# Optimization experiments

Measured on AMD Instinct MI355X. Metric: run time of the kernel, lower is better.

The kernel has to match this reference:

```python
import jax, jax.numpy as jnp
import numpy as np

# Edge-type spec: (src_node_type, dst_node_type); 0=argument, 1=evidence
REL_SPEC = ((0, 0), (1, 0), (0, 1))


def _hgt_layer(xs, edges, Wk, bk, Wq, bq, Wv, bv, a_rel, m_rel, p_rel, Wa, ba, skip):
    # xs: list of [N_t, C]; edges: tuple of [2, E] int arrays per edge type
    H, D = a_rel.shape[1], a_rel.shape[2]
    Ns = [x.shape[0] for x in xs]
    k = [(xs[t] @ Wk[t] + bk[t]).reshape(Ns[t], H, D) for t in range(len(xs))]
    q = [(xs[t] @ Wq[t] + bq[t]).reshape(Ns[t], H, D) for t in range(len(xs))]
    v = [(xs[t] @ Wv[t] + bv[t]).reshape(Ns[t], H, D) for t in range(len(xs))]
    scale = 1.0 / jnp.sqrt(jnp.asarray(D, xs[0].dtype))
    agg = [jnp.zeros((n, H, D), xs[0].dtype) for n in Ns]
    for r, (s, d) in enumerate(REL_SPEC):
        src, dst = edges[r][0], edges[r][1]
        # relation-specific key/message transforms, per edge: [E, H, D]
        k_e = jnp.einsum('ehd,hdf->ehf', k[s][src], a_rel[r])
        v_e = jnp.einsum('ehd,hdf->ehf', v[s][src], m_rel[r])
        alpha = jnp.einsum('ehd,ehd->eh', q[d][dst], k_e) * p_rel[r] * scale  # [E, H]
        # segment softmax over incoming edges of each destination node
        amax = jax.ops.segment_max(alpha, dst, num_segments=Ns[d])
        a_exp = jnp.exp(alpha - amax[dst])
        denom = jax.ops.segment_sum(a_exp, dst, num_segments=Ns[d])
        w = a_exp / jnp.maximum(denom[dst], 1e-16)
        agg[d] = agg[d] + jax.ops.segment_sum(v_e * w[..., None], dst, num_segments=Ns[d])
    out = []
    for t in range(len(xs)):
        o = jax.nn.gelu(agg[t].reshape(Ns[t], H * D), approximate=False) @ Wa[t] + ba[t]
        beta = jax.nn.sigmoid(skip[t])
        out.append(beta * o + (1.0 - beta) * xs[t])
    return out


def setup_inputs() -> dict:
    key = jax.random.key(0)
    N_ARG, N_EV, F_IN, C, H, L, E = 50000, 50000, 64, 128, 8, 2, 500000
    D = C // H
    R, T = 3, 2  # edge types, node types
    ks = jax.random.split(key, 20)
    s_in = 1.0 / np.sqrt(F_IN)
    s_c = 1.0 / np.sqrt(C)
    s_d = 1.0 / np.sqrt(D)
    inp = {
        'x_arg': jax.random.normal(ks[0], (N_ARG, F_IN), jnp.float32),
        'x_ev': jax.random.normal(ks[1], (N_EV, F_IN), jnp.float32),
        'edge_aa': jax.random.randint(ks[2], (2, E), 0, N_ARG, jnp.int32),
        'edge_ea': jax.random.randint(ks[3], (2, E), 0, N_EV, jnp.int32),
        'edge_ae': jax.random.randint(ks[4], (2, E), 0, N_ARG, jnp.int32),
        'Win_arg': jax.random.normal(ks[5], (F_IN, C), jnp.float32) * s_in,
        'bin_arg': jnp.zeros((C,), jnp.float32),
        'Win_ev': jax.random.normal(ks[6], (F_IN, C), jnp.float32) * s_in,
        'bin_ev': jnp.zeros((C,), jnp.float32),
        'Wk': jax.random.normal(ks[7], (L, T, C, C), jnp.float32) * s_c,
        'bk': jnp.zeros((L, T, C), jnp.float32),
        'Wq': jax.random.normal(ks[8], (L, T, C, C), jnp.float32) * s_c,
        'bq': jnp.zeros((L, T, C), jnp.float32),
        'Wv': jax.random.normal(ks[9], (L, T, C, C), jnp.float32) * s_c,
        'bv': jnp.zeros((L, T, C), jnp.float32),
        'a_rel': jax.random.normal(ks[10], (L, R, H, D, D), jnp.float32) * s_d,
        'm_rel': jax.random.normal(ks[11], (L, R, H, D, D), jnp.float32) * s_d,
        'p_rel': jnp.ones((L, R, H), jnp.float32),
        'Wa': jax.random.normal(ks[12], (L, T, C, C), jnp.float32) * s_c,
        'ba': jnp.zeros((L, T, C), jnp.float32),
        'skip': jnp.ones((L, T), jnp.float32),
        'Wc1': jax.random.normal(ks[13], (C, C), jnp.float32) * s_c,
        'bc1': jnp.zeros((C,), jnp.float32),
        'Wc2': jax.random.normal(ks[14], (C, 1), jnp.float32) * s_c,
        'bc2': jnp.zeros((1,), jnp.float32),
    }
    return inp


def reference(x_arg, x_ev, edge_aa, edge_ea, edge_ae, Win_arg, bin_arg, Win_ev, bin_ev,
              Wk, bk, Wq, bq, Wv, bv, a_rel, m_rel, p_rel, Wa, ba, skip,
              Wc1, bc1, Wc2, bc2):
    # type-specific input projections + relu
    h = [jax.nn.relu(x_arg @ Win_arg + bin_arg), jax.nn.relu(x_ev @ Win_ev + bin_ev)]
    edges = (edge_aa, edge_ea, edge_ae)
    for l in range(Wk.shape[0]):
        h = _hgt_layer(h, edges, Wk[l], bk[l], Wq[l], bq[l], Wv[l], bv[l],
                       a_rel[l], m_rel[l], p_rel[l], Wa[l], ba[l], skip[l])
    g = jnp.mean(h[0], axis=0, keepdims=True)  # [1, C]
    z = jax.nn.relu(g @ Wc1 + bc1)
    return jax.nn.sigmoid(z @ Wc2 + bc2)  # [1, 1]
```

## Files before the change

kernel.cpp:

```cpp
#include <hip/hip_runtime.h>
#include <hip/hip_fp8.h>
#include <math.h>

typedef __attribute__((ext_vector_type(8))) short short8v;
typedef __attribute__((ext_vector_type(4))) float f32x4;
typedef __attribute__((ext_vector_type(2))) float f32x2;

__device__ __forceinline__ float bf2f(unsigned short u) {
    union { unsigned int i; float f; } x; x.i = ((unsigned int)u) << 16; return x.f;
}
__device__ __forceinline__ unsigned short f2bf(float f) {
    union { float f; unsigned int i; } x; x.f = f;
    unsigned int r = x.i + 0x7fffu + ((x.i >> 16) & 1u);
    return (unsigned short)(r >> 16);
}
__device__ __forceinline__ unsigned int pk_bf16(float lo, float hi) {
    unsigned int r;
    asm("v_cvt_pk_bf16_f32 %0, %1, %2" : "=v"(r) : "v"(lo), "v"(hi));
    return r;
}
__device__ __forceinline__ unsigned int pk_fp8x4(float v0, float v1, float v2, float v3) {
    int pk = __builtin_amdgcn_cvt_pk_fp8_f32(v0, v1, 0, false);
    pk = __builtin_amdgcn_cvt_pk_fp8_f32(v2, v3, pk, true);
    return (unsigned int)pk;
}
__device__ __forceinline__ float gelu_exact(float x) {
    return 0.5f * x * (1.0f + erff(x * 0.70710678118654752f));
}

template <int K, int MODE, int ASRC>
__device__ __forceinline__ void gemm_body(
    const void* __restrict__ Aptr, const unsigned short* __restrict__ BT,
    const float* __restrict__ bias, unsigned short* __restrict__ Cout, int M,
    const unsigned short* __restrict__ hprev, const float* __restrict__ skipp, int blk) {
    __shared__ short As[128 * K];
    const int tid = threadIdx.x;
    const int row0 = blk * 128;
    const int CH = K / 8;

#pragma unroll
    for (int i = 0; i < (128 * CH) / 256; ++i) {
        int idx = tid + i * 256;
        int r = idx / CH, c = idx % CH;
        int gr = row0 + r;
        if (ASRC == 0) {
            short8v val = {0, 0, 0, 0, 0, 0, 0, 0};
            if (gr < M)
                val = *reinterpret_cast<const short8v*>(
                    (const unsigned short*)Aptr + (size_t)gr * K + c * 8);
            if (MODE == 2) {
                float fv[8];
#pragma unroll
                for (int u = 0; u < 8; ++u) fv[u] = gelu_exact(bf2f((unsigned short)val[u]));
                uint4 uu;
                uu.x = pk_bf16(fv[0], fv[1]);
                uu.y = pk_bf16(fv[2], fv[3]);
                uu.z = pk_bf16(fv[4], fv[5]);
                uu.w = pk_bf16(fv[6], fv[7]);
                *reinterpret_cast<uint4*>((char*)As + r * (2 * K) +
                                          ((c * 16) ^ ((r & 7) << 4))) = uu;
            } else {
                *reinterpret_cast<short8v*>((char*)As + r * (2 * K) +
                                            ((c * 16) ^ ((r & 7) << 4))) = val;
            }
        } else {
            uint4 u = make_uint4(0u, 0u, 0u, 0u);
            if (gr < M) {
                const float* Af = (const float*)Aptr;
                float4 f0 = *reinterpret_cast<const float4*>(Af + (size_t)gr * K + c * 8);
                float4 f1 = *reinterpret_cast<const float4*>(Af + (size_t)gr * K + c * 8 + 4);
                u.x = pk_bf16(f0.x, f0.y);
                u.y = pk_bf16(f0.z, f0.w);
                u.z = pk_bf16(f1.x, f1.y);
                u.w = pk_bf16(f1.z, f1.w);
            }
            *reinterpret_cast<uint4*>((char*)As + r * (2 * K) + ((c * 16) ^ ((r & 7) << 4))) = u;
        }
    }
    __syncthreads();

    const int lane = tid & 63, wid = tid >> 6;
    const int wr = wid >> 1, wc = wid & 1;
    const int lr = lane & 15, lg = lane >> 4;
    const int swz = (lr & 7) << 4;
    const unsigned short* bbase = BT + (size_t)(wc * 64 + lr) * K + lg * 8;
    f32x4 acc[4][4];
    f32x4 z4 = {0.f, 0.f, 0.f, 0.f};
#pragma unroll
    for (int mi = 0; mi < 4; ++mi)
#pragma unroll
        for (int ni = 0; ni < 4; ++ni) acc[mi][ni] = z4;

#pragma unroll
    for (int ks = 0; ks < K / 32; ++ks) {
        int kc = ks * 64 + lg * 16;
        short8v a[4], b[4];
#pragma unroll
        for (int ni = 0; ni < 4; ++ni)
            b[ni] = *reinterpret_cast<const short8v*>(bbase + (size_t)ni * 16 * K + ks * 32);
#pragma unroll
        for (int mi = 0; mi < 4; ++mi) {
            int r = wr * 64 + mi * 16 + lr;
            a[mi] = *reinterpret_cast<const short8v*>((char*)As + r * (2 * K) + (kc ^ swz));
        }
#pragma unroll
        for (int mi = 0; mi < 4; ++mi)
#pragma unroll
            for (int ni = 0; ni < 4; ++ni)
                acc[mi][ni] =
                    __builtin_amdgcn_mfma_f32_16x16x32_bf16(b[ni], a[mi], acc[mi][ni], 0, 0, 0);
    }

    float beta = 0.f;
    if (MODE == 2) beta = 1.f / (1.f + expf(-skipp[0]));
#pragma unroll
    for (int mi = 0; mi < 4; ++mi) {
        int gr = row0 + wr * 64 + mi * 16 + lr;
        if (gr >= M) continue;
#pragma unroll
        for (int ni = 0; ni < 4; ++ni) {
            int col0 = wc * 64 + ni * 16 + lg * 4;
            float4 bv = *reinterpret_cast<const float4*>(bias + col0);
            float v0 = acc[mi][ni][0] + bv.x;
            float v1 = acc[mi][ni][1] + bv.y;
            float v2 = acc[mi][ni][2] + bv.z;
            float v3 = acc[mi][ni][3] + bv.w;
            if (MODE == 1) {
                v0 = fmaxf(v0, 0.f); v1 = fmaxf(v1, 0.f);
                v2 = fmaxf(v2, 0.f); v3 = fmaxf(v3, 0.f);
            }
            if (MODE == 2) {
                ushort4 hp = *reinterpret_cast<const ushort4*>(hprev + (size_t)gr * 128 + col0);
                float ob = 1.f - beta;
                v0 = beta * v0 + ob * bf2f(hp.x);
                v1 = beta * v1 + ob * bf2f(hp.y);
                v2 = beta * v2 + ob * bf2f(hp.z);
                v3 = beta * v3 + ob * bf2f(hp.w);
            }
            uint2 us;
            us.x = pk_bf16(v0, v1);
            us.y = pk_bf16(v2, v3);
            *reinterpret_cast<uint2*>(Cout + (size_t)gr * 128 + col0) = us;
        }
    }
}

template <int K, int MODE, int ASRC>
__global__ __launch_bounds__(256) void gemm_dual(
    const void* A0, const unsigned short* BT0, const float* b0, unsigned short* C0, int M0,
    const unsigned short* hp0, const float* sk0,
    const void* A1, const unsigned short* BT1, const float* b1, unsigned short* C1, int M1,
    const unsigned short* hp1, const float* sk1, int nb0) {
    if ((int)blockIdx.x < nb0)
        gemm_body<K, MODE, ASRC>(A0, BT0, b0, C0, M0, hp0, sk0, blockIdx.x);
    else
        gemm_body<K, MODE, ASRC>(A1, BT1, b1, C1, M1, hp1, sk1, blockIdx.x - nb0);
}

struct QKVJobs {
    const unsigned short* BT[5];
    const float* bias[5];
    unsigned short* outBf[5];
    unsigned char* outF8[5];
    int f8off[5];
};

template <int NB>
__device__ __forceinline__ void qkv_body(short* __restrict__ As,
                                         const unsigned short* __restrict__ A,
                                         const QKVJobs& J, int M, int blk) {
    const int tid = threadIdx.x;
    const int row0 = blk * 128;

#pragma unroll
    for (int i = 0; i < 8; ++i) {
        int idx = tid + i * 256;
        int r = idx >> 4, c = idx & 15;
        int gr = row0 + r;
        short8v val = {0, 0, 0, 0, 0, 0, 0, 0};
        if (gr < M) val = *reinterpret_cast<const short8v*>(A + (size_t)gr * 128 + c * 8);
        *reinterpret_cast<short8v*>((char*)As + r * 256 + ((c * 16) ^ ((r & 7) << 4))) = val;
    }
    __syncthreads();

    const int lane = tid & 63, wid = tid >> 6;
    const int wr = wid >> 1, wc = wid & 1;
    const int lr = lane & 15, lg = lane >> 4;
    const int swz = (lr & 7) << 4;

    short8v a[4][4];
#pragma unroll
    for (int ks = 0; ks < 4; ++ks) {
        int kc = ks * 64 + lg * 16;
#pragma unroll
        for (int mi = 0; mi < 4; ++mi) {
            int r = wr * 64 + mi * 16 + lr;
            a[ks][mi] = *reinterpret_cast<const short8v*>((char*)As + r * 256 + (kc ^ swz));
        }
    }

#pragma unroll
    for (int m = 0; m < NB; ++m) {
        const unsigned short* bbase = J.BT[m] + (size_t)(wc * 64 + lr) * 128 + lg * 8;
        f32x4 acc[4][4];
        f32x4 z4 = {0.f, 0.f, 0.f, 0.f};
#pragma unroll
        for (int mi = 0; mi < 4; ++mi)
#pragma unroll
            for (int ni = 0; ni < 4; ++ni) acc[mi][ni] = z4;

#pragma unroll
        for (int ks = 0; ks < 4; ++ks) {
            short8v b[4];
#pragma unroll
            for (int ni = 0; ni < 4; ++ni)
                b[ni] = *reinterpret_cast<const short8v*>(bbase + (size_t)ni * 16 * 128 + ks * 32);
#pragma unroll
            for (int mi = 0; mi < 4; ++mi)
#pragma unroll
                for (int ni = 0; ni < 4; ++ni)
                    acc[mi][ni] = __builtin_amdgcn_mfma_f32_16x16x32_bf16(b[ni], a[ks][mi],
                                                                          acc[mi][ni], 0, 0, 0);
        }

        unsigned short* outBf = J.outBf[m];
        unsigned char* outF8 = J.outF8[m];
        int off = J.f8off[m];
        const float* bias = J.bias[m];
#pragma unroll
        for (int mi = 0; mi < 4; ++mi) {
            int gr = row0 + wr * 64 + mi * 16 + lr;
            if (gr >= M) continue;
#pragma unroll
            for (int ni = 0; ni < 4; ++ni) {
                int col0 = wc * 64 + ni * 16 + lg * 4;
                float4 bv = *reinterpret_cast<const float4*>(bias + col0);
                float v0 = acc[mi][ni][0] + bv.x;
                float v1 = acc[mi][ni][1] + bv.y;
                float v2 = acc[mi][ni][2] + bv.z;
                float v3 = acc[mi][ni][3] + bv.w;
                if (outBf) {
                    uint2 us;
                    us.x = pk_bf16(v0, v1);
                    us.y = pk_bf16(v2, v3);
                    *reinterpret_cast<uint2*>(outBf + (size_t)gr * 128 + col0) = us;
                } else {
                    *reinterpret_cast<unsigned int*>(outF8 + (size_t)gr * 256 + off + col0) =
                        pk_fp8x4(v0, v1, v2, v3);
                }
            }
        }
    }
}

__global__ __launch_bounds__(256) void gemm_qkv2(const unsigned short* A0, QKVJobs J0, int M0,
                                                 int nb0, const unsigned short* A1,
                                                 QKVJobs J1, int M1) {
    __shared__ short As[128 * 128];
    if ((int)blockIdx.x < nb0) qkv_body<5>(As, A0, J0, M0, blockIdx.x);
    else qkv_body<3>(As, A1, J1, M1, blockIdx.x - nb0);
}

__global__ void convT_kernel(const float* __restrict__ Win0, const float* __restrict__ Win1,
                             const float* __restrict__ Wq, const float* __restrict__ Wa,
                             unsigned short* __restrict__ winT, unsigned short* __restrict__ wqT,
                             unsigned short* __restrict__ waT, int nmat) {
    int gid = blockIdx.x * 256 + threadIdx.x;
    if (gid < 2 * 8192) {
        int m = gid >> 13, idx = gid & 8191;
        int n = idx >> 6, k = idx & 63;
        const float* W = m ? Win1 : Win0;
        winT[gid] = f2bf(W[(size_t)k * 128 + n]);
        return;
    }
    int g = gid - 2 * 8192;
    if (g < nmat * 16384) {
        int mat = g >> 14, idx = g & 16383;
        int n = idx >> 7, k = idx & 127;
        wqT[g] = f2bf(Wq[(size_t)mat * 16384 + (size_t)k * 128 + n]);
        return;
    }
    g -= nmat * 16384;
    if (g < nmat * 16384) {
        int mat = g >> 14, idx = g & 16383;
        int n = idx >> 7, k = idx & 127;
        waT[g] = f2bf(Wa[(size_t)mat * 16384 + (size_t)k * 128 + n]);
    }
}

__global__ void fold_kernel(const float* __restrict__ Wk, const float* __restrict__ bk,
                            const float* __restrict__ Wv, const float* __restrict__ bv,
                            const float* __restrict__ a_rel, const float* __restrict__ m_rel,
                            unsigned short* __restrict__ wfT, float* __restrict__ bfold, int L) {
    const int RSarr[3] = {0, 1, 0};
    int gid = blockIdx.x * 256 + threadIdx.x;
    int NW = L * 6 * 16384;
    if (gid < NW) {
        int fold = gid >> 14, idx = gid & 16383;
        int col = idx >> 7, i = idx & 127;
        int kv = fold & 1, lr = fold >> 1, l = lr / 3, r = lr % 3;
        int s = RSarr[r];
        const float* W = (kv ? Wv : Wk) + (size_t)(l * 2 + s) * 16384;
        const float* rel = (kv ? m_rel : a_rel) + (size_t)(l * 3 + r) * 2048;
        int hh = col >> 4, f = col & 15;
        float sacc = 0.f;
#pragma unroll
        for (int d = 0; d < 16; ++d)
            sacc += W[(size_t)i * 128 + hh * 16 + d] * rel[hh * 256 + d * 16 + f];
        wfT[gid] = f2bf(sacc);
        return;
    }
    int g = gid - NW;
    if (g >= L * 6 * 128) return;
    int fold = g >> 7, col = g & 127;
    int kv = fold & 1, lr = fold >> 1, l = lr / 3, r = lr % 3;
    int s = RSarr[r];
    const float* b = (kv ? bv : bk) + (size_t)(l * 2 + s) * 128;
    const float* rel = (kv ? m_rel : a_rel) + (size_t)(l * 3 + r) * 2048;
    int hh = col >> 4, f = col & 15;
    float sacc = 0.f;
#pragma unroll
    for (int d = 0; d < 16; ++d) sacc += b[hh * 16 + d] * rel[hh * 256 + d * 16 + f];
    bfold[fold * 128 + col] = sacc;
}

struct Csr3 {
    const int* src[3];
    const int* dst[3];
    int E[3];
    int* cnt;
    int* texcl;
    int* bsums;
    int* indptr[3];
    int* ssrc[3];
    int Nd[3];
    int nb[3];
    int stride;
};

__global__ void hist3_kernel(Csr3 P, int Etot) {
    int gid = blockIdx.x * 256 + threadIdx.x;
    if (gid >= Etot) return;
    int r = 0, off = gid;
    if (off >= P.E[0]) { off -= P.E[0]; r = 1; if (off >= P.E[1]) { off -= P.E[1]; r = 2; } }
    atomicAdd(&P.cnt[r * P.stride + P.dst[r][off]], 1);
}

__global__ __launch_bounds__(1024) void scanA3_kernel(Csr3 P) {
    __shared__ int s[1024];
    int b = blockIdx.x, r = 0;
    while (b >= P.nb[r]) { b -= P.nb[r]; ++r; }
    const int* cnt = P.cnt + r * P.stride;
    int* texcl = P.texcl + r * P.stride;
    int n = P.Nd[r];
    int t = threadIdx.x;
    int gid = b * 1024 + t;
    int x = (gid < n) ? cnt[gid] : 0;
    s[t] = x;
    __syncthreads();
    for (int off = 1; off < 1024; off <<= 1) {
        int v = (t >= off) ? s[t - off] : 0;
        __syncthreads();
        s[t] += v;
        __syncthreads();
    }
    if (gid < n) texcl[gid] = s[t] - x;
    if (t == 1023) P.bsums[r * 64 + b] = s[1023];
}

__global__ void scanB3_kernel(Csr3 P) {
    int r = blockIdx.x;
    if (threadIdx.x == 0) {
        int run = 0;
        for (int i = 0; i < P.nb[r]; ++i) {
            int t = P.bsums[r * 64 + i];
            P.bsums[r * 64 + i] = run;
            run += t;
        }
    }
}

__global__ __launch_bounds__(1024) void scanC3_kernel(Csr3 P) {
    int b = blockIdx.x, r = 0;
    while (b >= P.nb[r]) { b -= P.nb[r]; ++r; }
    int n = P.Nd[r];
    int gid = b * 1024 + threadIdx.x;
    if (gid < n) {
        int v = P.texcl[r * P.stride + gid] + P.bsums[r * 64 + b];
        P.indptr[r][gid] = v;
        P.cnt[r * P.stride + gid] = v;
    }
    if (gid == 0) P.indptr[r][n] = P.E[r];
}

__global__ void scatter3_kernel(Csr3 P, int Etot) {
    int gid = blockIdx.x * 256 + threadIdx.x;
    if (gid >= Etot) return;
    int r = 0, off = gid;
    if (off >= P.E[0]) { off -= P.E[0]; r = 1; if (off >= P.E[1]) { off -= P.E[1]; r = 2; } }
    int d = P.dst[r][off];
    int p = atomicAdd(&P.cnt[r * P.stride + d], 1);
    P.ssrc[r][p] = P.src[r][off];
}

__global__ void gcur_init_kernel(Csr3 P, int* __restrict__ gcur) {
    int t = threadIdx.x;
    if (t >= 192) return;
    int r = t >> 6, b = t & 63;
    int nbk = (P.Nd[r] + 1023) >> 10;
    gcur[t] = (b < nbk) ? P.indptr[r][b << 10] : 0;
}

#define PA_TILE 4096
#define PA_BLKS 64
__global__ __launch_bounds__(256) void partA_kernel(Csr3 P, unsigned int* __restrict__ pb0,
                                                    unsigned int* __restrict__ pb1,
                                                    unsigned int* __restrict__ pb2,
                                                    int* __restrict__ gcur) {
    unsigned int* pbuf[3] = {pb0, pb1, pb2};
    const int r = blockIdx.x / PA_BLKS;
    const int blk = blockIdx.x % PA_BLKS;
    const int tid = threadIdx.x;
    const int* __restrict__ srcp = P.src[r];
    const int* __restrict__ dstp = P.dst[r];
    const int E = P.E[r];
    unsigned int* __restrict__ out = pbuf[r];
    __shared__ unsigned int stage[PA_TILE];
    __shared__ unsigned char bkt[PA_TILE];
    __shared__ int lcnt[64], lofs[64], lbase[64];

    for (int t0 = blk * PA_TILE; t0 < E; t0 += PA_BLKS * PA_TILE) {
        int cnt = E - t0;
        if (cnt > PA_TILE) cnt = PA_TILE;
        if (tid < 64) lcnt[tid] = 0;
        __syncthreads();
        unsigned int pk[16];
        int lp[16];
#pragma unroll
        for (int j = 0; j < 16; ++j) {
            int i = tid + j * 256;
            if (i < cnt) {
                int s = srcp[t0 + i];
                int d = dstp[t0 + i];
                pk[j] = ((unsigned int)d << 16) | (unsigned int)s;
                lp[j] = atomicAdd(&lcnt[d >> 10], 1);
            }
        }
        __syncthreads();
        if (tid == 0) {
            int run = 0;
            for (int b = 0; b < 64; ++b) { lofs[b] = run; run += lcnt[b]; }
        }
        __syncthreads();
        if (tid < 64 && lcnt[tid] > 0) lbase[tid] = atomicAdd(&gcur[r * 64 + tid], lcnt[tid]);
        __syncthreads();
#pragma unroll
        for (int j = 0; j < 16; ++j) {
            int i = tid + j * 256;
            if (i < cnt) {
                int b = pk[j] >> 26;
                int sp = lofs[b] + lp[j];
                stage[sp] = pk[j];
                bkt[sp] = (unsigned char)b;
            }
        }
        __syncthreads();
        for (int k = tid; k < cnt; k += 256) {
            int b = bkt[k];
            out[lbase[b] + (k - lofs[b])] = stage[k];
        }
        __syncthreads();
    }
}

__global__ __launch_bounds__(256) void partB_kernel(Csr3 P, const unsigned int* __restrict__ pb0,
                                                    const unsigned int* __restrict__ pb1,
                                                    const unsigned int* __restrict__ pb2) {
    const unsigned int* pbuf[3] = {pb0, pb1, pb2};
    int r = blockIdx.x >> 6, b = blockIdx.x & 63;
    int Nd = P.Nd[r];
    int nbk = (Nd + 1023) >> 10;
    if (b >= nbk) return;
    int d1 = (b + 1) << 10;
    if (d1 > Nd) d1 = Nd;
    int lo = P.indptr[r][b << 10];
    int hi = P.indptr[r][d1];
    const unsigned int* __restrict__ pin = pbuf[r];
    int* __restrict__ cursor = P.cnt + r * P.stride;
    int* __restrict__ out = P.ssrc[r];
    for (int i = lo + (int)threadIdx.x; i < hi; i += 256) {
        unsigned int pk = pin[i];
        int d = pk >> 16;
        int p = atomicAdd(&cursor[d], 1);
        out[p] = (int)(pk & 0xffffu);
    }
}

__device__ __forceinline__ void proc4(uint4 Kw, uint4 Vw, const float qf[16], float ps,
                                      bool valid, float& ssum, float acc[16]) {
    float kx[16];
    {
        f32x2 p0 = __builtin_amdgcn_cvt_pk_f32_fp8(Kw.x, false);
        f32x2 p1 = __builtin_amdgcn_cvt_pk_f32_fp8(Kw.x, true);
        f32x2 p2 = __builtin_amdgcn_cvt_pk_f32_fp8(Kw.y, false);
        f32x2 p3 = __builtin_amdgcn_cvt_pk_f32_fp8(Kw.y, true);
        f32x2 p4 = __builtin_amdgcn_cvt_pk_f32_fp8(Kw.z, false);
        f32x2 p5 = __builtin_amdgcn_cvt_pk_f32_fp8(Kw.z, true);
        f32x2 p6 = __builtin_amdgcn_cvt_pk_f32_fp8(Kw.w, false);
        f32x2 p7 = __builtin_amdgcn_cvt_pk_f32_fp8(Kw.w, true);
        kx[0] = p0[0]; kx[1] = p0[1]; kx[2] = p1[0]; kx[3] = p1[1];
        kx[4] = p2[0]; kx[5] = p2[1]; kx[6] = p3[0]; kx[7] = p3[1];
        kx[8] = p4[0]; kx[9] = p4[1]; kx[10] = p5[0]; kx[11] = p5[1];
        kx[12] = p6[0]; kx[13] = p6[1]; kx[14] = p7[0]; kx[15] = p7[1];
    }
    float t = 0.f;
#pragma unroll
    for (int j = 0; j < 16; ++j) t = fmaf(qf[j], kx[j], t);
    float e = fminf(fmaxf(t * ps, -40.f), 40.f);
    float w = valid ? exp2f(e) : 0.f;
    ssum += w;
    float vx[16];
    {
        f32x2 p0 = __builtin_amdgcn_cvt_pk_f32_fp8(Vw.x, false);
        f32x2 p1 = __builtin_amdgcn_cvt_pk_f32_fp8(Vw.x, true);
        f32x2 p2 = __builtin_amdgcn_cvt_pk_f32_fp8(Vw.y, false);
        f32x2 p3 = __builtin_amdgcn_cvt_pk_f32_fp8(Vw.y, true);
        f32x2 p4 = __builtin_amdgcn_cvt_pk_f32_fp8(Vw.z, false);
        f32x2 p5 = __builtin_amdgcn_cvt_pk_f32_fp8(Vw.z, true);
        f32x2 p6 = __builtin_amdgcn_cvt_pk_f32_fp8(Vw.w, false);
        f32x2 p7 = __builtin_amdgcn_cvt_pk_f32_fp8(Vw.w, true);
        vx[0] = p0[0]; vx[1] = p0[1]; vx[2] = p1[0]; vx[3] = p1[1];
        vx[4] = p2[0]; vx[5] = p2[1]; vx[6] = p3[0]; vx[7] = p3[1];
        vx[8] = p4[0]; vx[9] = p4[1]; vx[10] = p5[0]; vx[11] = p5[1];
        vx[12] = p6[0]; vx[13] = p6[1]; vx[14] = p7[0]; vx[15] = p7[1];
    }
#pragma unroll
    for (int j = 0; j < 16; ++j) acc[j] = fmaf(w, vx[j], acc[j]);
}

__device__ __forceinline__ void slot_load(const unsigned char* __restrict__ kv,
                                          const int* __restrict__ ss, int beg, int n, int j4,
                                          int lq, int lhb, int eslot, int hoff, int& bat,
                                          uint4& Kw, uint4& Vw) {
    if ((j4 & 31) == 0) bat = (j4 + lq < n) ? ss[beg + j4 + lq] : 0;
    int s = __shfl(bat, lhb + ((j4 + eslot) & 31));
    const unsigned char* bp = kv + (size_t)s * 256 + hoff;
    Kw = *reinterpret_cast<const uint4*>(bp);
    Vw = *reinterpret_cast<const uint4*>(bp + 128);
}

__global__ __launch_bounds__(256) void attn_fused(
    const unsigned short* __restrict__ q0, const unsigned short* __restrict__ q1,
    const unsigned char* __restrict__ kvA, const unsigned char* __restrict__ kvB,
    const unsigned char* __restrict__ kvC,
    const int* __restrict__ ipA, const int* __restrict__ ssA,
    const int* __restrict__ ipB, const int* __restrict__ ssB,
    const int* __restrict__ ipC, const int* __restrict__ ssC,
    unsigned short* __restrict__ agg0, unsigned short* __restrict__ agg1,
    const float* __restrict__ prA, const float* __restrict__ prB,
    const float* __restrict__ prC, int N0, int N1) {
    const int wave = (blockIdx.x * blockDim.x + threadIdx.x) >> 6;
    const int lane = threadIdx.x & 63;
    const int lq = lane & 31;
    const int lhb = lane & 32;
    const int h = lq & 7;
    const int eslot = lq >> 3;
    const int hoff = h * 16;
    const float LOG2E = 1.4426950408889634f;
    const int P0 = (N0 + 1) >> 1;
    const int P1 = (N1 + 1) >> 1;
    if (wave >= P0 + P1) return;

    if (wave < P0) {
        int dst = wave * 2 + (lhb >> 5);
        bool act = dst < N0;
        float qf[16];
        int b1 = 0, n1 = 0, b2 = 0, n2 = 0;
        if (act) {
            short8v qv0 = *reinterpret_cast<const short8v*>(q0 + (size_t)dst * 128 + hoff);
            short8v qv1 = *reinterpret_cast<const short8v*>(q0 + (size_t)dst * 128 + hoff + 8);
#pragma unroll
            for (int j = 0; j < 8; ++j) {
                qf[j] = bf2f((unsigned short)qv0[j]);
                qf[8 + j] = bf2f((unsigned short)qv1[j]);
            }
            b1 = ipA[dst]; n1 = ipA[dst + 1] - b1;
            b2 = ipB[dst]; n2 = ipB[dst + 1] - b2;
        } else {
#pragma unroll
            for (int j = 0; j < 16; ++j) qf[j] = 0.f;
        }
        float ps1 = prA[h] * 0.25f * LOG2E;
        float ps2 = prB[h] * 0.25f * LOG2E;
        float ssum1 = 0.f, ssum2 = 0.f;
        float acc1[16], acc2[16];
#pragma unroll
        for (int j = 0; j < 16; ++j) { acc1[j] = 0.f; acc2[j] = 0.f; }
        int it1 = (n1 + 3) >> 2, it2 = (n2 + 3) >> 2;
        int itm = (it1 > it2) ? it1 : it2;
        int bat1 = 0, bat2 = 0;
        uint4 cK1{}, cV1{}, cK2{}, cV2{};
        if (it1 > 0) slot_load(kvA, ssA, b1, n1, 0, lq, lhb, eslot, hoff, bat1, cK1, cV1);
        if (it2 > 0) slot_load(kvB, ssB, b2, n2, 0, lq, lhb, eslot, hoff, bat2, cK2, cV2);
        for (int i = 0; i < itm; ++i) {
            uint4 nK1{}, nV1{}, nK2{}, nV2{};
            if (i + 1 < it1)
                slot_load(kvA, ssA, b1, n1, (i + 1) * 4, lq, lhb, eslot, hoff, bat1, nK1, nV1);
            if (i + 1 < it2)
                slot_load(kvB, ssB, b2, n2, (i + 1) * 4, lq, lhb, eslot, hoff, bat2, nK2, nV2);
            if (i < it1) proc4(cK1, cV1, qf, ps1, (i * 4 + eslot) < n1, ssum1, acc1);
            if (i < it2) proc4(cK2, cV2, qf, ps2, (i * 4 + eslot) < n2, ssum2, acc2);
            cK1 = nK1; cV1 = nV1; cK2 = nK2; cV2 = nV2;
        }
#pragma unroll
        for (int j = 0; j < 16; ++j) {
            acc1[j] += __shfl_xor(acc1[j], 8);
            acc1[j] += __shfl_xor(acc1[j], 16);
            acc2[j] += __shfl_xor(acc2[j], 8);
            acc2[j] += __shfl_xor(acc2[j], 16);
        }
        ssum1 += __shfl_xor(ssum1, 8);
        ssum1 += __shfl_xor(ssum1, 16);
        ssum2 += __shfl_xor(ssum2, 8);
        ssum2 += __shfl_xor(ssum2, 16);
        if (act && eslot == 0) {
            float i1 = 1.f / fmaxf(ssum1, 1e-16f);
            float i2 = 1.f / fmaxf(ssum2, 1e-16f);
            float v[16];
#pragma unroll
            for (int j = 0; j < 16; ++j) v[j] = acc1[j] * i1 + acc2[j] * i2;
            unsigned short* op = agg0 + (size_t)dst * 128 + hoff;
            uint4 w0, w1;
            w0.x = pk_bf16(v[0], v[1]);  w0.y = pk_bf16(v[2], v[3]);
            w0.z = pk_bf16(v[4], v[5]);  w0.w = pk_bf16(v[6], v[7]);
            w1.x = pk_bf16(v[8], v[9]);  w1.y = pk_bf16(v[10], v[11]);
            w1.z = pk_bf16(v[12], v[13]); w1.w = pk_bf16(v[14], v[15]);
            *reinterpret_cast<uint4*>(op) = w0;
            *reinterpret_cast<uint4*>(op + 8) = w1;
        }
    } else {
        int dst = (wave - P0) * 2 + (lhb >> 5);
        bool act = dst < N1;
        float qf[16];
        int b1 = 0, n1 = 0;
        if (act) {
            short8v qv0 = *reinterpret_cast<const short8v*>(q1 + (size_t)dst * 128 + hoff);
            short8v qv1 = *reinterpret_cast<const short8v*>(q1 + (size_t)dst * 128 + hoff + 8);
#pragma unroll
            for (int j = 0; j < 8; ++j) {
                qf[j] = bf2f((unsigned short)qv0[j]);
                qf[8 + j] = bf2f((unsigned short)qv1[j]);
            }
            b1 = ipC[dst]; n1 = ipC[dst + 1] - b1;
        } else {
#pragma unroll
            for (int j = 0; j < 16; ++j) qf[j] = 0.f;
        }
        float ps1 = prC[h] * 0.25f * LOG2E;
        float ssum1 = 0.f;
        float acc1[16];
#pragma unroll
        for (int j = 0; j < 16; ++j) acc1[j] = 0.f;
        int it1 = (n1 + 3) >> 2;
        int bat1 = 0;
        uint4 cK1{}, cV1{};
        if (it1 > 0) slot_load(kvC, ssC, b1, n1, 0, lq, lhb, eslot, hoff, bat1, cK1, cV1);
        for (int i = 0; i < it1; ++i) {
            uint4 nK1{}, nV1{};
            if (i + 1 < it1)
                slot_load(kvC, ssC, b1, n1, (i + 1) * 4, lq, lhb, eslot, hoff, bat1, nK1, nV1);
            proc4(cK1, cV1, qf, ps1, (i * 4 + eslot) < n1, ssum1, acc1);
            cK1 = nK1; cV1 = nV1;
        }
#pragma unroll
        for (int j = 0; j < 16; ++j) {
            acc1[j] += __shfl_xor(acc1[j], 8);
            acc1[j] += __shfl_xor(acc1[j], 16);
        }
        ssum1 += __shfl_xor(ssum1, 8);
        ssum1 += __shfl_xor(ssum1, 16);
        if (act && eslot == 0) {
            float i1 = 1.f / fmaxf(ssum1, 1e-16f);
            float v[16];
#pragma unroll
            for (int j = 0; j < 16; ++j) v[j] = acc1[j] * i1;
            unsigned short* op = agg1 + (size_t)dst * 128 + hoff;
            uint4 w0, w1;
            w0.x = pk_bf16(v[0], v[1]);  w0.y = pk_bf16(v[2], v[3]);
            w0.z = pk_bf16(v[4], v[5]);  w0.w = pk_bf16(v[6], v[7]);
            w1.x = pk_bf16(v[8], v[9]);  w1.y = pk_bf16(v[10], v[11]);
            w1.z = pk_bf16(v[12], v[13]); w1.w = pk_bf16(v[14], v[15]);
            *reinterpret_cast<uint4*>(op) = w0;
            *reinterpret_cast<uint4*>(op + 8) = w1;
        }
    }
}

__global__ void colsum_kernel(const unsigned short* __restrict__ h, float* __restrict__ gsum,
                              int M) {
    int c = threadIdx.x;
    float s = 0.f;
    for (int r = blockIdx.x; r < M; r += gridDim.x) s += bf2f(h[(size_t)r * 128 + c]);
    atomicAdd(&gsum[c], s);
}

__global__ void final_kernel(const float* __restrict__ gsum, const float* __restrict__ Wc1,
                             const float* __restrict__ bc1, const float* __restrict__ Wc2,
                             const float* __restrict__ bc2, float* __restrict__ out,
                             float invM) {
    __shared__ float g[128];
    __shared__ float red[128];
    int t = threadIdx.x;
    g[t] = gsum[t] * invM;
    __syncthreads();
    float acc = bc1[t];
    for (int k = 0; k < 128; ++k) acc += g[k] * Wc1[k * 128 + t];
    float zv = fmaxf(acc, 0.f);
    red[t] = zv * Wc2[t];
    __syncthreads();
    for (int off = 64; off > 0; off >>= 1) {
        if (t < off) red[t] += red[t + off];
        __syncthreads();
    }
    if (t == 0) out[0] = 1.f / (1.f + expf(-(red[0] + bc2[0])));
}

extern "C" void kernel_launch(void* const* d_in, const int* in_sizes, int n_in,
                              void* d_out, int out_size, void* d_ws, size_t ws_size,
                              hipStream_t stream) {
    const float* x[2] = {(const float*)d_in[0], (const float*)d_in[1]};
    const int* edges[3] = {(const int*)d_in[2], (const int*)d_in[3], (const int*)d_in[4]};
    const float* Win[2] = {(const float*)d_in[5], (const float*)d_in[7]};
    const float* bin[2] = {(const float*)d_in[6], (const float*)d_in[8]};
    const float* Wk = (const float*)d_in[9];
    const float* bk = (const float*)d_in[10];
    const float* Wq = (const float*)d_in[11];
    const float* bq = (const float*)d_in[12];
    const float* Wv = (const float*)d_in[13];
    const float* bv = (const float*)d_in[14];
    const float* a_rel = (const float*)d_in[15];
    const float* m_rel = (const float*)d_in[16];
    const float* p_rel = (const float*)d_in[17];
    const float* Wa = (const float*)d_in[18];
    const float* ba = (const float*)d_in[19];
    const float* skip = (const float*)d_in[20];
    const float* Wc1 = (const float*)d_in[21];
    const float* bc1 = (const float*)d_in[22];
    const float* Wc2 = (const float*)d_in[23];
    const float* bc2 = (const float*)d_in[24];

    const int N0 = in_sizes[0] / 64;
    const int N1 = in_sizes[1] / 64;
    const int L = in_sizes[9] / (2 * 128 * 128);
    const int Ns[2] = {N0, N1};
    const int RD[3] = {0, 0, 1};
    const int Nmax = (N0 > N1) ? N0 : N1;

    char* p = (char*)d_ws;
    auto alloc = [&](size_t bytes) -> void* {
        void* r = (void*)p;
        p += (bytes + 255) & ~(size_t)255;
        return r;
    };
    unsigned short* h[2];
    unsigned short* q[2];
    unsigned short* agg[2];
    h[0] = (unsigned short*)alloc((size_t)N0 * 128 * 2);
    h[1] = (unsigned short*)alloc((size_t)N1 * 128 * 2);
    q[0] = (unsigned short*)alloc((size_t)N0 * 128 * 2);
    q[1] = (unsigned short*)alloc((size_t)N1 * 128 * 2);
    agg[0] = (unsigned short*)alloc((size_t)N0 * 128 * 2);
    agg[1] = (unsigned short*)alloc((size_t)N1 * 128 * 2);
    unsigned char* kv8[3];
    for (int r = 0; r < 3; ++r) kv8[r] = (unsigned char*)alloc((size_t)Nmax * 256);
    int* indptr[3];
    int* ssrc[3];
    int Er[3];
    for (int r = 0; r < 3; ++r) {
        Er[r] = in_sizes[2 + r] / 2;
        indptr[r] = (int*)alloc((size_t)(Ns[RD[r]] + 1) * 4);
        ssrc[r] = (int*)alloc((size_t)Er[r] * 4);
    }
    unsigned int* pbuf[3];
    for (int r = 0; r < 3; ++r) pbuf[r] = (unsigned int*)alloc((size_t)Er[r] * 4);
    int* cnt3 = (int*)alloc((size_t)3 * Nmax * 4);
    int* texcl3 = (int*)alloc((size_t)3 * Nmax * 4);
    int* bsums3 = (int*)alloc(3 * 64 * 4);
    int* gcur = (int*)alloc(3 * 64 * 4);
    unsigned short* winT = (unsigned short*)alloc(2 * 8192 * 2);
    unsigned short* wqT = (unsigned short*)alloc((size_t)L * 2 * 16384 * 2);
    unsigned short* waT = (unsigned short*)alloc((size_t)L * 2 * 16384 * 2);
    unsigned short* wfT = (unsigned short*)alloc((size_t)L * 6 * 16384 * 2);
    float* bfold = (float*)alloc((size_t)L * 6 * 128 * 4);
    float* gsum = (float*)alloc(128 * 4);

    {
        int nmat = L * 2;
        int convN = 2 * 8192 + 2 * nmat * 16384;
        convT_kernel<<<(convN + 255) / 256, 256, 0, stream>>>(Win[0], Win[1], Wq, Wa, winT, wqT,
                                                              waT, nmat);
        int foldN = L * 6 * 16384 + L * 6 * 128;
        fold_kernel<<<(foldN + 255) / 256, 256, 0, stream>>>(Wk, bk, Wv, bv, a_rel, m_rel, wfT,
                                                             bfold, L);
    }

    {
        Csr3 P;
        int Etot = 0;
        int nbTot = 0;
        for (int r = 0; r < 3; ++r) {
            P.src[r] = edges[r];
            P.dst[r] = edges[r] + Er[r];
            P.E[r] = Er[r];
            P.indptr[r] = indptr[r];
            P.ssrc[r] = ssrc[r];
            P.Nd[r] = Ns[RD[r]];
            P.nb[r] = (P.Nd[r] + 1023) / 1024;
            Etot += Er[r];
            nbTot += P.nb[r];
        }
        P.cnt = cnt3;
        P.texcl = texcl3;
        P.bsums = bsums3;
        P.stride = Nmax;
        hipMemsetAsync(cnt3, 0, (size_t)3 * Nmax * 4, stream);
        hist3_kernel<<<(Etot + 255) / 256, 256, 0, stream>>>(P, Etot);
        scanA3_kernel<<<nbTot, 1024, 0, stream>>>(P);
        scanB3_kernel<<<3, 64, 0, stream>>>(P);
        scanC3_kernel<<<nbTot, 1024, 0, stream>>>(P);
        if (Nmax <= 65536) {
            gcur_init_kernel<<<1, 256, 0, stream>>>(P, gcur);
            partA_kernel<<<3 * PA_BLKS, 256, 0, stream>>>(P, pbuf[0], pbuf[1], pbuf[2], gcur);
            partB_kernel<<<3 * 64, 256, 0, stream>>>(P, pbuf[0], pbuf[1], pbuf[2]);
        } else {
            scatter3_kernel<<<(Etot + 255) / 256, 256, 0, stream>>>(P, Etot);
        }
    }

    const int nb0 = (N0 + 127) / 128, nb1 = (N1 + 127) / 128;

    gemm_dual<64, 1, 1><<<nb0 + nb1, 256, 0, stream>>>(
        x[0], winT, bin[0], h[0], N0, nullptr, nullptr,
        x[1], winT + 8192, bin[1], h[1], N1, nullptr, nullptr, nb0);

    for (int l = 0; l < L; ++l) {
        {
            QKVJobs J0{};
            J0.BT[0] = wqT + (size_t)(l * 2 + 0) * 16384;
            J0.bias[0] = bq + (size_t)(l * 2 + 0) * 128;
            J0.outBf[0] = q[0]; J0.outF8[0] = nullptr; J0.f8off[0] = 0;
            int fk0 = (l * 3 + 0) * 2, fk2 = (l * 3 + 2) * 2;
            J0.BT[1] = wfT + (size_t)fk0 * 16384;       J0.bias[1] = bfold + (size_t)fk0 * 128;
            J0.outBf[1] = nullptr; J0.outF8[1] = kv8[0]; J0.f8off[1] = 0;
            J0.BT[2] = wfT + (size_t)(fk0 + 1) * 16384; J0.bias[2] = bfold + (size_t)(fk0 + 1) * 128;
            J0.outBf[2] = nullptr; J0.outF8[2] = kv8[0]; J0.f8off[2] = 128;
            J0.BT[3] = wfT + (size_t)fk2 * 16384;       J0.bias[3] = bfold + (size_t)fk2 * 128;
            J0.outBf[3] = nullptr; J0.outF8[3] = kv8[2]; J0.f8off[3] = 0;
            J0.BT[4] = wfT + (size_t)(fk2 + 1) * 16384; J0.bias[4] = bfold + (size_t)(fk2 + 1) * 128;
            J0.outBf[4] = nullptr; J0.outF8[4] = kv8[2]; J0.f8off[4] = 128;
            QKVJobs J1{};
            J1.BT[0] = wqT + (size_t)(l * 2 + 1) * 16384;
            J1.bias[0] = bq + (size_t)(l * 2 + 1) * 128;
            J1.outBf[0] = q[1]; J1.outF8[0] = nullptr; J1.f8off[0] = 0;
            int fk1 = (l * 3 + 1) * 2;
            J1.BT[1] = wfT + (size_t)fk1 * 16384;       J1.bias[1] = bfold + (size_t)fk1 * 128;
            J1.outBf[1] = nullptr; J1.outF8[1] = kv8[1]; J1.f8off[1] = 0;
            J1.BT[2] = wfT + (size_t)(fk1 + 1) * 16384; J1.bias[2] = bfold + (size_t)(fk1 + 1) * 128;
            J1.outBf[2] = nullptr; J1.outF8[2] = kv8[1]; J1.f8off[2] = 128;
            gemm_qkv2<<<nb0 + nb1, 256, 0, stream>>>(h[0], J0, N0, nb0, h[1], J1, N1);
        }
        {
            int waves = ((N0 + 1) >> 1) + ((N1 + 1) >> 1);
            attn_fused<<<(waves + 3) / 4, 256, 0, stream>>>(
                q[0], q[1], kv8[0], kv8[1], kv8[2], indptr[0], ssrc[0], indptr[1], ssrc[1],
                indptr[2], ssrc[2], agg[0], agg[1], p_rel + (size_t)(l * 3 + 0) * 8,
                p_rel + (size_t)(l * 3 + 1) * 8, p_rel + (size_t)(l * 3 + 2) * 8, N0, N1);
        }
        gemm_dual<128, 2, 0><<<nb0 + nb1, 256, 0, stream>>>(
            agg[0], waT + (size_t)(l * 2 + 0) * 16384, ba + (size_t)(l * 2 + 0) * 128, h[0], N0,
            h[0], skip + (size_t)(l * 2 + 0),
            agg[1], waT + (size_t)(l * 2 + 1) * 16384, ba + (size_t)(l * 2 + 1) * 128, h[1], N1,
            h[1], skip + (size_t)(l * 2 + 1), nb0);
    }

    hipMemsetAsync(gsum, 0, 128 * 4, stream);
    colsum_kernel<<<512, 128, 0, stream>>>(h[0], gsum, N0);
    final_kernel<<<1, 128, 0, stream>>>(gsum, Wc1, bc1, Wc2, bc2, (float*)d_out,
                                        1.0f / (float)N0);
}
```

Measured before the change: 571.4 us.

## Replace global histogram and scan CSR build with bucketed counting sort

For the small-graph path, CSR construction no longer runs a full per-node global histogram with atomics followed by a three-pass scan. It counts edges per 1024-node bucket with shared-memory atomics, scans the 64 bucket totals in a single thread, and partitions edges by bucket. Each partB block then builds its own local histogram and scan in shared memory to write indptr, and scatters sources using shared-memory atomics. This removes the large memset and the global atomic traffic, at the cost of one extra pass over the dst array and a serial scan kernel.

```diff
diff --git a/kernel.cpp b/kernel.cpp
--- a/kernel.cpp
+++ b/kernel.cpp
@@ -403,12 +403,39 @@
     P.ssrc[r][p] = P.src[r][off];
 }
 
-__global__ void gcur_init_kernel(Csr3 P, int* __restrict__ gcur) {
-    int t = threadIdx.x;
-    if (t >= 192) return;
-    int r = t >> 6, b = t & 63;
-    int nbk = (P.Nd[r] + 1023) >> 10;
-    gcur[t] = (b < nbk) ? P.indptr[r][b << 10] : 0;
+#define CA_TILE 4096
+__global__ __launch_bounds__(256) void countA_kernel(Csr3 P, int* __restrict__ gbkt) {
+    const int r = blockIdx.x >> 6;
+    const int blk = blockIdx.x & 63;
+    const int tid = threadIdx.x;
+    const int* __restrict__ dstp = P.dst[r];
+    const int E = P.E[r];
+    __shared__ int lc[64];
+    for (int t0 = blk * CA_TILE; t0 < E; t0 += 64 * CA_TILE) {
+        int cnt = E - t0;
+        if (cnt > CA_TILE) cnt = CA_TILE;
+        if (tid < 64) lc[tid] = 0;
+        __syncthreads();
+        for (int i = tid; i < cnt; i += 256) atomicAdd(&lc[dstp[t0 + i] >> 10], 1);
+        __syncthreads();
+        if (tid < 64 && lc[tid] > 0) atomicAdd(&gbkt[r * 65 + tid], lc[tid]);
+        __syncthreads();
+    }
+}
+
+__global__ void scanG_kernel(int* __restrict__ gbkt, int* __restrict__ gcur) {
+    if (threadIdx.x == 0) {
+        for (int r = 0; r < 3; ++r) {
+            int run = 0;
+            for (int b = 0; b < 64; ++b) {
+                int t = gbkt[r * 65 + b];
+                gbkt[r * 65 + b] = run;
+                gcur[r * 64 + b] = run;
+                run += t;
+            }
+            gbkt[r * 65 + 64] = run;
+        }
+    }
 }
 
 #define PA_TILE 4096
@@ -473,26 +500,59 @@
     }
 }
 
-__global__ __launch_bounds__(256) void partB_kernel(Csr3 P, const unsigned int* __restrict__ pb0,
-                                                    const unsigned int* __restrict__ pb1,
-                                                    const unsigned int* __restrict__ pb2) {
+__global__ __launch_bounds__(256) void partB2_kernel(Csr3 P, const unsigned int* __restrict__ pb0,
+                                                     const unsigned int* __restrict__ pb1,
+                                                     const unsigned int* __restrict__ pb2,
+                                                     const int* __restrict__ gbkt) {
     const unsigned int* pbuf[3] = {pb0, pb1, pb2};
     int r = blockIdx.x >> 6, b = blockIdx.x & 63;
     int Nd = P.Nd[r];
     int nbk = (Nd + 1023) >> 10;
     if (b >= nbk) return;
-    int d1 = (b + 1) << 10;
+    int d0 = b << 10;
+    int d1 = d0 + 1024;
     if (d1 > Nd) d1 = Nd;
-    int lo = P.indptr[r][b << 10];
-    int hi = P.indptr[r][d1];
+    int lo = gbkt[r * 65 + b];
+    int hi = gbkt[r * 65 + b + 1];
     const unsigned int* __restrict__ pin = pbuf[r];
-    int* __restrict__ cursor = P.cnt + r * P.stride;
+    int* __restrict__ indptr = P.indptr[r];
     int* __restrict__ out = P.ssrc[r];
-    for (int i = lo + (int)threadIdx.x; i < hi; i += 256) {
+    const int tid = threadIdx.x;
+    __shared__ int cnt[1024];
+    __shared__ int exc[1024];
+    __shared__ int ps[256];
+
+    for (int i = tid; i < 1024; i += 256) cnt[i] = 0;
+    __syncthreads();
+    for (int i = lo + tid; i < hi; i += 256)
+        atomicAdd(&cnt[(pin[i] >> 16) & 1023], 1);
+    __syncthreads();
+    int base = tid * 4;
+    int s0 = cnt[base], s1 = cnt[base + 1], s2 = cnt[base + 2], s3 = cnt[base + 3];
+    int tsum = s0 + s1 + s2 + s3;
+    ps[tid] = tsum;
+    __syncthreads();
+    for (int off = 1; off < 256; off <<= 1) {
+        int v = (tid >= off) ? ps[tid - off] : 0;
+        __syncthreads();
+        ps[tid] += v;
+        __syncthreads();
+    }
+    int texc = ps[tid] - tsum;
+    exc[base] = texc;
+    exc[base + 1] = texc + s0;
+    exc[base + 2] = texc + s0 + s1;
+    exc[base + 3] = texc + s0 + s1 + s2;
+    __syncthreads();
+    for (int i = tid; i < (d1 - d0); i += 256) indptr[d0 + i] = lo + exc[i];
+    if (b == nbk - 1 && tid == 0) indptr[Nd] = P.E[r];
+    for (int i = tid; i < 1024; i += 256) cnt[i] = exc[i];
+    __syncthreads();
+    for (int i = lo + tid; i < hi; i += 256) {
         unsigned int pk = pin[i];
-        int d = pk >> 16;
-        int p = atomicAdd(&cursor[d], 1);
-        out[p] = (int)(pk & 0xffffu);
+        int dl = (pk >> 16) & 1023;
+        int p = atomicAdd(&cnt[dl], 1);
+        out[lo + p] = (int)(pk & 0xffffu);
     }
 }
 
@@ -786,6 +846,7 @@
     int* cnt3 = (int*)alloc((size_t)3 * Nmax * 4);
     int* texcl3 = (int*)alloc((size_t)3 * Nmax * 4);
     int* bsums3 = (int*)alloc(3 * 64 * 4);
+    int* gbkt = (int*)alloc(3 * 65 * 4);
     int* gcur = (int*)alloc(3 * 64 * 4);
     unsigned short* winT = (unsigned short*)alloc(2 * 8192 * 2);
     unsigned short* wqT = (unsigned short*)alloc((size_t)L * 2 * 16384 * 2);
@@ -823,16 +884,18 @@
         P.texcl = texcl3;
         P.bsums = bsums3;
         P.stride = Nmax;
-        hipMemsetAsync(cnt3, 0, (size_t)3 * Nmax * 4, stream);
-        hist3_kernel<<<(Etot + 255) / 256, 256, 0, stream>>>(P, Etot);
-        scanA3_kernel<<<nbTot, 1024, 0, stream>>>(P);
-        scanB3_kernel<<<3, 64, 0, stream>>>(P);
-        scanC3_kernel<<<nbTot, 1024, 0, stream>>>(P);
         if (Nmax <= 65536) {
-            gcur_init_kernel<<<1, 256, 0, stream>>>(P, gcur);
+            hipMemsetAsync(gbkt, 0, 3 * 65 * 4, stream);
+            countA_kernel<<<3 * 64, 256, 0, stream>>>(P, gbkt);
+            scanG_kernel<<<1, 64, 0, stream>>>(gbkt, gcur);
             partA_kernel<<<3 * PA_BLKS, 256, 0, stream>>>(P, pbuf[0], pbuf[1], pbuf[2], gcur);
-            partB_kernel<<<3 * 64, 256, 0, stream>>>(P, pbuf[0], pbuf[1], pbuf[2]);
+            partB2_kernel<<<3 * 64, 256, 0, stream>>>(P, pbuf[0], pbuf[1], pbuf[2], gbkt);
         } else {
+            hipMemsetAsync(cnt3, 0, (size_t)3 * Nmax * 4, stream);
+            hist3_kernel<<<(Etot + 255) / 256, 256, 0, stream>>>(P, Etot);
+            scanA3_kernel<<<nbTot, 1024, 0, stream>>>(P);
+            scanB3_kernel<<<3, 64, 0, stream>>>(P);
+            scanC3_kernel<<<nbTot, 1024, 0, stream>>>(P);
             scatter3_kernel<<<(Etot + 255) / 256, 256, 0, stream>>>(P, Etot);
         }
     }
```

Result: faster. 491.9 us (-13.9%).
